# Kernel tuning notes

Measured on AMD Instinct MI355X. Metric: run time of the kernel, lower is better.

The kernel has to match this reference:

```python
import jax, jax.numpy as jnp
import numpy as np

N = 50000
E = 1000000
FN = 16
FE = 8
H = 64
DH = 64
LN_EPS = 1e-5


def _layernorm(x, g, b):
    mu = jnp.mean(x, axis=-1, keepdims=True)
    var = jnp.var(x, axis=-1, keepdims=True)
    return (x - mu) * jax.lax.rsqrt(var + LN_EPS) * g + b


def setup_inputs() -> dict:
    key = jax.random.key(0)
    ks = jax.random.split(key, 24)

    def w(k, i, o):
        return jax.random.normal(k, (i, o), jnp.float32) / np.sqrt(i).astype(np.float32)

    inp = {}
    inp["x"] = jax.random.normal(ks[0], (N, FN), jnp.float32)
    inp["edge_index"] = jax.random.randint(ks[1], (2, E), 0, N, dtype=jnp.int32)
    inp["edge_attr"] = jax.random.normal(ks[2], (E, FE), jnp.float32)
    # layer 0 (in_dim = FN, residual is a Linear since FN != H)
    inp["l0_lin_w"] = w(ks[3], FE, FN); inp["l0_lin_b"] = jnp.zeros((FN,), jnp.float32)
    inp["l0_w1"] = w(ks[4], FN, H);    inp["l0_b1"] = jnp.zeros((H,), jnp.float32)
    inp["l0_w2"] = w(ks[5], H, H);     inp["l0_b2"] = jnp.zeros((H,), jnp.float32)
    inp["l0_ln_g"] = jnp.ones((H,), jnp.float32); inp["l0_ln_b"] = jnp.zeros((H,), jnp.float32)
    inp["l0_res_w"] = w(ks[6], FN, H); inp["l0_res_b"] = jnp.zeros((H,), jnp.float32)
    # layers 1, 2 (in_dim = H, residual = identity)
    for li, base in ((1, 7), (2, 11)):
        inp[f"l{li}_lin_w"] = w(ks[base], FE, H);   inp[f"l{li}_lin_b"] = jnp.zeros((H,), jnp.float32)
        inp[f"l{li}_w1"] = w(ks[base + 1], H, H);   inp[f"l{li}_b1"] = jnp.zeros((H,), jnp.float32)
        inp[f"l{li}_w2"] = w(ks[base + 2], H, H);   inp[f"l{li}_b2"] = jnp.zeros((H,), jnp.float32)
        inp[f"l{li}_ln_g"] = jnp.ones((H,), jnp.float32)
        inp[f"l{li}_ln_b"] = jnp.zeros((H,), jnp.float32)
    D_IN = 4 * H + FE
    inp["dec_w1"] = w(ks[20], D_IN, DH);    inp["dec_b1"] = jnp.zeros((DH,), jnp.float32)
    inp["dec_w2"] = w(ks[21], DH, DH // 2); inp["dec_b2"] = jnp.zeros((DH // 2,), jnp.float32)
    inp["dec_w3"] = w(ks[22], DH // 2, 1);  inp["dec_b3"] = jnp.zeros((1,), jnp.float32)
    return inp


def _block(x, src, dst, edge_attr, lin_w, lin_b, w1, b1, w2, b2, ln_g, ln_b, res):
    # GINEConv: message = ReLU(x_src + Lin(edge_attr)); sum-aggregate at dst; eps=0
    msg = jax.nn.relu(x[src] + edge_attr @ lin_w + lin_b)      # (E, D_in)
    aggr = jax.ops.segment_sum(msg, dst, num_segments=N)       # (N, D_in)
    h = jax.nn.relu((x + aggr) @ w1 + b1) @ w2 + b2            # GIN nn MLP -> (N, H)
    h = jax.nn.relu(h)                                         # dropout inactive (eval)
    return _layernorm(h + res, ln_g, ln_b)


def reference(x, edge_index, edge_attr,
              l0_lin_w, l0_lin_b, l0_w1, l0_b1, l0_w2, l0_b2, l0_ln_g, l0_ln_b, l0_res_w, l0_res_b,
              l1_lin_w, l1_lin_b, l1_w1, l1_b1, l1_w2, l1_b2, l1_ln_g, l1_ln_b,
              l2_lin_w, l2_lin_b, l2_w1, l2_b1, l2_w2, l2_b2, l2_ln_g, l2_ln_b,
              dec_w1, dec_b1, dec_w2, dec_b2, dec_w3, dec_b3):
    src, dst = edge_index[0], edge_index[1]
    h = _block(x, src, dst, edge_attr, l0_lin_w, l0_lin_b, l0_w1, l0_b1, l0_w2, l0_b2,
               l0_ln_g, l0_ln_b, x @ l0_res_w + l0_res_b)
    h = _block(h, src, dst, edge_attr, l1_lin_w, l1_lin_b, l1_w1, l1_b1, l1_w2, l1_b2,
               l1_ln_g, l1_ln_b, h)
    h = _block(h, src, dst, edge_attr, l2_lin_w, l2_lin_b, l2_w1, l2_b1, l2_w2, l2_b2,
               l2_ln_g, l2_ln_b, h)
    hs, hd = h[src], h[dst]                                    # (E, H) each
    z = jnp.concatenate([hs, hd, jnp.abs(hs - hd), hs * hd, edge_attr], axis=-1)  # (E, 4H+FE)
    z = jax.nn.relu(z @ dec_w1 + dec_b1)
    z = jax.nn.relu(z @ dec_w2 + dec_b2)
    return (z @ dec_w3 + dec_b3)[:, 0]                         # (E,)
```

## Files before the change

### kernel.cpp

```cpp
#include <hip/hip_runtime.h>

#define NN 50000
#define NE 1000000

constexpr float LN_EPS = 1e-5f;

typedef short bf16x8 __attribute__((ext_vector_type(8)));
typedef float f32x4 __attribute__((ext_vector_type(4)));
typedef uint uvec4 __attribute__((ext_vector_type(4)));
typedef uint uvec2 __attribute__((ext_vector_type(2)));

__device__ inline uint cvtpk(float a, float b) {
  uint r;
  asm("v_cvt_pk_bf16_f32 %0, %1, %2" : "=v"(r) : "v"(a), "v"(b));
  return r;
}
__device__ inline ushort cvt1(float a) {
  uint r;
  asm("v_cvt_pk_bf16_f32 %0, %1, %1" : "=v"(r) : "v"(a));
  return (ushort)r;
}
__device__ inline float bflo(uint u) { union { uint x; float f; } v; v.x = u << 16; return v.f; }
__device__ inline float bfhi(uint u) { union { uint x; float f; } v; v.x = u & 0xffff0000u; return v.f; }

__global__ __launch_bounds__(256) void hist_kernel(const int* __restrict__ ei,
                                                   int* __restrict__ cnt) {
  int e = blockIdx.x * 256 + threadIdx.x;
  if (e < NE) atomicAdd(&cnt[ei[NE + e]], 1);
}

__global__ __launch_bounds__(256) void scan1_kernel(const int* __restrict__ cnt,
                                                    int* __restrict__ off,
                                                    int* __restrict__ bsum) {
  __shared__ int sh[256];
  int t = threadIdx.x;
  int idx = blockIdx.x * 256 + t;
  int v = (idx < NN) ? cnt[idx] : 0;
  sh[t] = v;
  __syncthreads();
  for (int o = 1; o < 256; o <<= 1) {
    int xv = (t >= o) ? sh[t - o] : 0;
    __syncthreads();
    sh[t] += xv;
    __syncthreads();
  }
  if (idx <= NN) off[idx] = sh[t] - v;
  if (t == 255) bsum[blockIdx.x] = sh[255];
}

__global__ __launch_bounds__(256) void scan2_kernel(int* __restrict__ bsum, int nb) {
  __shared__ int sh[256];
  int t = threadIdx.x;
  int v = (t < nb) ? bsum[t] : 0;
  sh[t] = v;
  __syncthreads();
  for (int o = 1; o < 256; o <<= 1) {
    int xv = (t >= o) ? sh[t - o] : 0;
    __syncthreads();
    sh[t] += xv;
    __syncthreads();
  }
  if (t < nb) bsum[t] = sh[t] - v;
}

__global__ __launch_bounds__(256) void scan3_kernel(int* __restrict__ off,
                                                    const int* __restrict__ bsum,
                                                    int* __restrict__ cnt) {
  int idx = blockIdx.x * 256 + threadIdx.x;
  if (idx <= NN) off[idx] += bsum[blockIdx.x];
  if (idx < NN) cnt[idx] = 0;
}

__global__ __launch_bounds__(256) void scatter_kernel(
    const int* __restrict__ ei, const float* __restrict__ ea,
    const int* __restrict__ off, int* __restrict__ cur,
    int* __restrict__ ipos, int* __restrict__ srcp, int* __restrict__ dstp,
    ushort* __restrict__ eapb) {
  int e = blockIdx.x * 256 + threadIdx.x;
  if (e < NE) {
    int d = ei[NE + e];
    int s = ei[e];
    int p = off[d] + atomicAdd(&cur[d], 1);
    ipos[e] = p;
    srcp[p] = s;
    dstp[p] = d;
    const float* eaf = ea + (size_t)e * 8;
    f32x4 e0 = *(const f32x4*)(eaf);
    f32x4 e1 = *(const f32x4*)(eaf + 4);
    uvec4 u;
    u.x = cvtpk(e0.x, e0.y);
    u.y = cvtpk(e0.z, e0.w);
    u.z = cvtpk(e1.x, e1.y);
    u.w = cvtpk(e1.z, e1.w);
    __builtin_nontemporal_store(u, (uvec4*)(eapb + (size_t)p * 8));
  }
}

__global__ __launch_bounds__(256) void unperm_kernel(const float* __restrict__ tmp,
                                                     const int* __restrict__ ipos,
                                                     float* __restrict__ out) {
  int e = blockIdx.x * 256 + threadIdx.x;
  if (e < NE) out[e] = tmp[ipos[e]];
}

__device__ inline float lane_layernorm(float r, float g, float b) {
  float s = r;
#pragma unroll
  for (int m = 32; m >= 1; m >>= 1) s += __shfl_xor(s, m);
  float mu = s * (1.f / 64.f);
  float dv = r - mu;
  float v = dv * dv;
#pragma unroll
  for (int m = 32; m >= 1; m >>= 1) v += __shfl_xor(v, m);
  float var = v * (1.f / 64.f);
  return dv * rsqrtf(var + LN_EPS) * g + b;
}

__global__ __launch_bounds__(256) void layer0_fused(
    const float* __restrict__ x, float* __restrict__ hout,
    ushort* __restrict__ houtbf,
    const ushort* __restrict__ eapb, const int* __restrict__ srcp,
    const int* __restrict__ off,
    const float* __restrict__ lw, const float* __restrict__ lb,
    const float* __restrict__ w1, const float* __restrict__ b1,
    const float* __restrict__ w2, const float* __restrict__ b2,
    const float* __restrict__ lng, const float* __restrict__ lnb,
    const float* __restrict__ rw, const float* __restrict__ rb) {
  int n = blockIdx.x * 4 + (threadIdx.x >> 6);
  int j = threadIdx.x & 63;
  int d = j & 15, slot = j >> 4;
  int start = off[n], end = off[n + 1];
  float lwv[8];
#pragma unroll
  for (int i = 0; i < 8; i++) lwv[i] = lw[i * 16 + d];
  float lbv = lb[d];
  float acc = 0.f;
  for (int base = start; base < end; base += 64) {
    int idx = base + j;
    int sl = (idx < end) ? srcp[idx] : 0;
    int c = min(end - base, 64);
    for (int i0 = 0; i0 < c; i0 += 4) {
      int i = i0 + slot;
      bool valid = i < c;
      int ii = i & 63;
      int s = __shfl(sl, ii);
      int pp = min(base + i0 + slot, NE - 1);
      float ev = bflo((uint)eapb[(size_t)pp * 8 + (d & 7)]);
      float xs = x[(size_t)s * 16 + d];
      float m = lbv + xs;
#pragma unroll
      for (int q = 0; q < 8; q++) m = fmaf(__shfl(ev, slot * 16 + q), lwv[q], m);
      m = fmaxf(m, 0.f);
      acc += valid ? m : 0.f;
    }
  }
  acc += __shfl_xor(acc, 16);
  acc += __shfl_xor(acc, 32);
  float xr = x[(size_t)n * 16 + d];
  float t = xr + acc;
  float q1 = b1[j];
#pragma unroll 4
  for (int k = 0; k < 16; k++) q1 = fmaf(__shfl(t, k), w1[k * 64 + j], q1);
  q1 = fmaxf(q1, 0.f);
  float h2 = b2[j];
  for (int k = 0; k < 64; k++) h2 = fmaf(__shfl(q1, k), w2[k * 64 + j], h2);
  h2 = fmaxf(h2, 0.f);
  float res = rb[j];
#pragma unroll 4
  for (int k = 0; k < 16; k++) res = fmaf(__shfl(xr, k), rw[k * 64 + j], res);
  float v = lane_layernorm(h2 + res, lng[j], lnb[j]);
  hout[(size_t)n * 64 + j] = v;
  houtbf[(size_t)n * 64 + j] = cvt1(v);
}

__device__ inline float edge8_msg(const ushort* __restrict__ hinb, int s, int j,
                                  uint ulo, uint uhi, uint vlo, uint vhi,
                                  const float* lwv, float lbv) {
  float hc = bflo((uint)hinb[(size_t)s * 64 + j]);
  float m = lbv + hc;
  m = fmaf(bflo(ulo), lwv[0], m);
  m = fmaf(bfhi(ulo), lwv[1], m);
  m = fmaf(bflo(uhi), lwv[2], m);
  m = fmaf(bfhi(uhi), lwv[3], m);
  m = fmaf(bflo(vlo), lwv[4], m);
  m = fmaf(bfhi(vlo), lwv[5], m);
  m = fmaf(bflo(vhi), lwv[6], m);
  m = fmaf(bfhi(vhi), lwv[7], m);
  return fmaxf(m, 0.f);
}

__global__ __launch_bounds__(256) void layer_fused(
    const ushort* __restrict__ hinb, const float* __restrict__ hinf,
    float* __restrict__ houtf, ushort* __restrict__ houtbf,
    const ushort* __restrict__ eapb, const int* __restrict__ srcp,
    const int* __restrict__ off,
    const float* __restrict__ lw, const float* __restrict__ lb,
    const float* __restrict__ w1, const float* __restrict__ b1,
    const float* __restrict__ w2, const float* __restrict__ b2,
    const float* __restrict__ lng, const float* __restrict__ lnb) {
  int n = blockIdx.x * 4 + (threadIdx.x >> 6);
  int j = threadIdx.x & 63;
  int start = __builtin_amdgcn_readfirstlane(off[n]);
  int end = __builtin_amdgcn_readfirstlane(off[n + 1]);
  float lwv[8];
#pragma unroll
  for (int i = 0; i < 8; i++) lwv[i] = lw[i * 64 + j];
  float lbv = lb[j];
  float acc = 0.f;
  int p = start;
  for (; p + 8 <= end; p += 8) {
    const uvec4* ip = (const uvec4*)(srcp + p);
    uvec4 I0 = __builtin_nontemporal_load(ip + 0);
    uvec4 I1 = __builtin_nontemporal_load(ip + 1);
    int s0 = __builtin_amdgcn_readfirstlane((int)I0.x);
    int s1 = __builtin_amdgcn_readfirstlane((int)I0.y);
    int s2 = __builtin_amdgcn_readfirstlane((int)I0.z);
    int s3 = __builtin_amdgcn_readfirstlane((int)I0.w);
    int s4 = __builtin_amdgcn_readfirstlane((int)I1.x);
    int s5 = __builtin_amdgcn_readfirstlane((int)I1.y);
    int s6 = __builtin_amdgcn_readfirstlane((int)I1.z);
    int s7 = __builtin_amdgcn_readfirstlane((int)I1.w);
    const uvec4* ep = (const uvec4*)(eapb + (size_t)p * 8);
    uint ua[8][4];
#pragma unroll
    for (int i = 0; i < 8; i++) {
      uvec4 E = __builtin_nontemporal_load(ep + i);
      ua[i][0] = __builtin_amdgcn_readfirstlane(E.x);
      ua[i][1] = __builtin_amdgcn_readfirstlane(E.y);
      ua[i][2] = __builtin_amdgcn_readfirstlane(E.z);
      ua[i][3] = __builtin_amdgcn_readfirstlane(E.w);
    }
    acc += edge8_msg(hinb, s0, j, ua[0][0], ua[0][1], ua[0][2], ua[0][3], lwv, lbv);
    acc += edge8_msg(hinb, s1, j, ua[1][0], ua[1][1], ua[1][2], ua[1][3], lwv, lbv);
    acc += edge8_msg(hinb, s2, j, ua[2][0], ua[2][1], ua[2][2], ua[2][3], lwv, lbv);
    acc += edge8_msg(hinb, s3, j, ua[3][0], ua[3][1], ua[3][2], ua[3][3], lwv, lbv);
    acc += edge8_msg(hinb, s4, j, ua[4][0], ua[4][1], ua[4][2], ua[4][3], lwv, lbv);
    acc += edge8_msg(hinb, s5, j, ua[5][0], ua[5][1], ua[5][2], ua[5][3], lwv, lbv);
    acc += edge8_msg(hinb, s6, j, ua[6][0], ua[6][1], ua[6][2], ua[6][3], lwv, lbv);
    acc += edge8_msg(hinb, s7, j, ua[7][0], ua[7][1], ua[7][2], ua[7][3], lwv, lbv);
  }
  for (; p < end; p++) {
    int s = __builtin_amdgcn_readfirstlane(srcp[p]);
    uvec4 E = __builtin_nontemporal_load((const uvec4*)(eapb + (size_t)p * 8));
    uint e0 = __builtin_amdgcn_readfirstlane(E.x);
    uint e1 = __builtin_amdgcn_readfirstlane(E.y);
    uint e2 = __builtin_amdgcn_readfirstlane(E.z);
    uint e3 = __builtin_amdgcn_readfirstlane(E.w);
    acc += edge8_msg(hinb, s, j, e0, e1, e2, e3, lwv, lbv);
  }
  float hv = __builtin_nontemporal_load(&hinf[(size_t)n * 64 + j]);
  float t = hv + acc;
  float q1 = b1[j];
  for (int k = 0; k < 64; k++) q1 = fmaf(__shfl(t, k), w1[k * 64 + j], q1);
  q1 = fmaxf(q1, 0.f);
  float h2 = b2[j];
  for (int k = 0; k < 64; k++) h2 = fmaf(__shfl(q1, k), w2[k * 64 + j], h2);
  h2 = fmaxf(h2, 0.f);
  float v = lane_layernorm(h2 + hv, lng[j], lnb[j]);
  if (houtf) houtf[(size_t)n * 64 + j] = v;
  houtbf[(size_t)n * 64 + j] = cvt1(v);
}

__global__ __launch_bounds__(256) void prep_kernel(
    const float* __restrict__ w1, const float* __restrict__ w2,
    ushort* __restrict__ w1f, ushort* __restrict__ w2f) {
  int t = blockIdx.x * 256 + threadIdx.x;
  if (t < 18432) {
    int j = t & 7, lane = (t >> 3) & 63, f = t >> 9;
    int k = (f >> 2) * 32 + ((lane >> 4) * 8) + j;
    int n = (f & 3) * 16 + (lane & 15);
    float v = (k < 264) ? w1[k * 64 + n] : 0.f;
    w1f[t] = cvt1(v);
  } else {
    int t2 = t - 18432;
    int j = t2 & 7, lane = (t2 >> 3) & 63, f = t2 >> 9;
    int k = (f >> 1) * 32 + ((lane >> 4) * 8) + j;
    int n = (f & 1) * 16 + (lane & 15);
    w2f[t2] = cvt1(w2[k * 32 + n]);
  }
}

#define YS 72
#define NBLK 15625
#define BPX 1954

__device__ inline void absmul(bf16x8 a, bf16x8 b, bf16x8& dd, bf16x8& pp) {
  union U { bf16x8 v; uvec4 u; } ua, ub, ud, up;
  ua.v = a; ub.v = b;
#pragma unroll
  for (int i = 0; i < 4; i++) {
    float a0 = bflo(ua.u[i]), a1 = bfhi(ua.u[i]);
    float b0 = bflo(ub.u[i]), b1 = bfhi(ub.u[i]);
    ud.u[i] = cvtpk(fabsf(a0 - b0), fabsf(a1 - b1));
    up.u[i] = cvtpk(a0 * b0, a1 * b1);
  }
  dd = ud.v; pp = up.v;
}

__global__ __launch_bounds__(128, 4) void decoder_kernel(
    const ushort* __restrict__ hb,
    const int* __restrict__ srcp, const int* __restrict__ dstp,
    const ushort* __restrict__ eapb,
    const ushort* __restrict__ w1f, const ushort* __restrict__ w2f,
    const float* __restrict__ b1, const float* __restrict__ b2,
    const float* __restrict__ w3, const float* __restrict__ b3,
    float* __restrict__ tmp) {
  __shared__ ushort ybuf[2][32 * YS];
  const int w = threadIdx.x >> 6, l = threadIdx.x & 63;
  const int sub = l & 15, quad = l >> 4;
  int bb = (blockIdx.x & 7) * BPX + (blockIdx.x >> 3);
  if (bb >= NBLK) return;
  const int g = bb * 2 + w;
  ushort* Y = ybuf[w];

  int s32 = __builtin_nontemporal_load(&srcp[g * 32 + (l & 31)]);
  int d32 = __builtin_nontemporal_load(&dstp[g * 32 + (l & 31)]);

  bf16x8 alo[2], ahi[2], blo[2], bhi[2];
#pragma unroll
  for (int m = 0; m < 2; m++) {
    int sA = __shfl(s32, m * 16 + sub);
    int dA = __shfl(d32, m * 16 + sub);
    const ushort* pa = hb + (size_t)sA * 64 + quad * 8;
    const ushort* pb = hb + (size_t)dA * 64 + quad * 8;
    alo[m] = *(const bf16x8*)pa;
    ahi[m] = *(const bf16x8*)(pa + 32);
    blo[m] = *(const bf16x8*)pb;
    bhi[m] = *(const bf16x8*)(pb + 32);
  }
  bf16x8 eaf0 = (bf16x8){0, 0, 0, 0, 0, 0, 0, 0};
  bf16x8 eaf1 = (bf16x8){0, 0, 0, 0, 0, 0, 0, 0};
  if (quad == 0) {
    eaf0 = *(const bf16x8*)&eapb[((size_t)g * 32 + sub) * 8];
    eaf1 = *(const bf16x8*)&eapb[((size_t)g * 32 + 16 + sub) * 8];
  }

  float b1v[4];
#pragma unroll
  for (int t = 0; t < 4; t++) b1v[t] = b1[t * 16 + sub];
  float b2v0 = b2[sub], b2v1 = b2[16 + sub];
  float w3v0 = w3[sub], w3v1 = w3[16 + sub];
  float b3v = b3[0];

  f32x4 acc[2][4];
#pragma unroll
  for (int m = 0; m < 2; m++)
#pragma unroll
    for (int t = 0; t < 4; t++) acc[m][t] = (f32x4){0.f, 0.f, 0.f, 0.f};

#define MF(sB, f0, f1)                                                        \
  {                                                                           \
    _Pragma("unroll") for (int t = 0; t < 4; t++) {                           \
      bf16x8 bfv = ((const bf16x8*)w1f)[((sB)*4 + t) * 64 + l];               \
      acc[0][t] = __builtin_amdgcn_mfma_f32_16x16x32_bf16(f0, bfv, acc[0][t], \
                                                          0, 0, 0);           \
      acc[1][t] = __builtin_amdgcn_mfma_f32_16x16x32_bf16(f1, bfv, acc[1][t], \
                                                          0, 0, 0);           \
    }                                                                         \
  }

  {
    bf16x8 dlo0, plo0, dlo1, plo1;
    absmul(alo[0], blo[0], dlo0, plo0);
    absmul(alo[1], blo[1], dlo1, plo1);
    MF(0, alo[0], alo[1]);
    MF(2, blo[0], blo[1]);
    MF(4, dlo0, dlo1);
    MF(6, plo0, plo1);
  }
  {
    bf16x8 dhi0, phi0, dhi1, phi1;
    absmul(ahi[0], bhi[0], dhi0, phi0);
    absmul(ahi[1], bhi[1], dhi1, phi1);
    MF(1, ahi[0], ahi[1]);
    MF(3, bhi[0], bhi[1]);
    MF(5, dhi0, dhi1);
    MF(7, phi0, phi1);
  }
  MF(8, eaf0, eaf1);
#undef MF

#pragma unroll
  for (int m = 0; m < 2; m++)
#pragma unroll
    for (int t = 0; t < 4; t++)
#pragma unroll
      for (int r = 0; r < 4; r++)
        Y[(m * 16 + quad * 4 + r) * YS + t * 16 + sub] =
            cvt1(fmaxf(acc[m][t][r] + b1v[t], 0.f));

  bf16x8 w2frag[4];
#pragma unroll
  for (int f = 0; f < 4; f++) w2frag[f] = ((const bf16x8*)w2f)[f * 64 + l];
  f32x4 acc2[2][2];
#pragma unroll
  for (int m = 0; m < 2; m++) {
    acc2[m][0] = (f32x4){0.f, 0.f, 0.f, 0.f};
    acc2[m][1] = (f32x4){0.f, 0.f, 0.f, 0.f};
#pragma unroll
    for (int ks = 0; ks < 2; ks++) {
      bf16x8 ya = *(const bf16x8*)&Y[(m * 16 + sub) * YS + ks * 32 + quad * 8];
      acc2[m][0] = __builtin_amdgcn_mfma_f32_16x16x32_bf16(ya, w2frag[ks * 2 + 0],
                                                           acc2[m][0], 0, 0, 0);
      acc2[m][1] = __builtin_amdgcn_mfma_f32_16x16x32_bf16(ya, w2frag[ks * 2 + 1],
                                                           acc2[m][1], 0, 0, 0);
    }
  }
#pragma unroll
  for (int m = 0; m < 2; m++)
#pragma unroll
    for (int r = 0; r < 4; r++) {
      float o = fmaxf(acc2[m][0][r] + b2v0, 0.f) * w3v0 +
                fmaxf(acc2[m][1][r] + b2v1, 0.f) * w3v1;
      o += __shfl_xor(o, 1);
      o += __shfl_xor(o, 2);
      o += __shfl_xor(o, 4);
      o += __shfl_xor(o, 8);
      if (sub == 0) tmp[g * 32 + m * 16 + quad * 4 + r] = o + b3v;
    }
}

extern "C" void kernel_launch(void* const* d_in, const int* in_sizes, int n_in,
                              void* d_out, int out_size, void* d_ws, size_t ws_size,
                              hipStream_t stream) {
  const float* x = (const float*)d_in[0];
  const int* ei = (const int*)d_in[1];
  const float* ea = (const float*)d_in[2];
  const float* l0_lin_w = (const float*)d_in[3];
  const float* l0_lin_b = (const float*)d_in[4];
  const float* l0_w1 = (const float*)d_in[5];
  const float* l0_b1 = (const float*)d_in[6];
  const float* l0_w2 = (const float*)d_in[7];
  const float* l0_b2 = (const float*)d_in[8];
  const float* l0_ln_g = (const float*)d_in[9];
  const float* l0_ln_b = (const float*)d_in[10];
  const float* l0_res_w = (const float*)d_in[11];
  const float* l0_res_b = (const float*)d_in[12];
  const float* dec_w1 = (const float*)d_in[29];
  const float* dec_b1 = (const float*)d_in[30];
  const float* dec_w2 = (const float*)d_in[31];
  const float* dec_b2 = (const float*)d_in[32];
  const float* dec_w3 = (const float*)d_in[33];
  const float* dec_b3 = (const float*)d_in[34];

  float* h_a = (float*)d_ws;
  float* h_b = h_a + (size_t)NN * 64;
  ushort* hbA = (ushort*)(h_b + (size_t)NN * 64);
  ushort* hbB = hbA + (size_t)NN * 64;
  int* ipos = (int*)(hbB + (size_t)NN * 64);
  int* srcp = ipos + NE;
  int* dstp = srcp + NE;
  float* tmp = (float*)(dstp + NE);
  int* off = (int*)(tmp + NE);
  int* cnt = off + (NN + 1);
  int* bsum = cnt + NN;
  ushort* w1f = (ushort*)(bsum + 256);
  ushort* w2f = w1f + 18432;
  ushort* eapb = w2f + 2048;

  const int EB = (NE + 255) / 256;
  const int SB = (NN + 256) / 256;

  hipMemsetAsync(cnt, 0, (size_t)NN * sizeof(int), stream);
  hist_kernel<<<EB, 256, 0, stream>>>(ei, cnt);
  scan1_kernel<<<SB, 256, 0, stream>>>(cnt, off, bsum);
  scan2_kernel<<<1, 256, 0, stream>>>(bsum, SB);
  scan3_kernel<<<SB, 256, 0, stream>>>(off, bsum, cnt);
  scatter_kernel<<<EB, 256, 0, stream>>>(ei, ea, off, cnt, ipos, srcp, dstp, eapb);

  layer0_fused<<<NN / 4, 256, 0, stream>>>(x, h_a, hbA, eapb, srcp, off,
                                           l0_lin_w, l0_lin_b, l0_w1, l0_b1,
                                           l0_w2, l0_b2, l0_ln_g, l0_ln_b,
                                           l0_res_w, l0_res_b);
  layer_fused<<<NN / 4, 256, 0, stream>>>(hbA, h_a, h_b, hbB, eapb, srcp, off,
                                          (const float*)d_in[13], (const float*)d_in[14],
                                          (const float*)d_in[15], (const float*)d_in[16],
                                          (const float*)d_in[17], (const float*)d_in[18],
                                          (const float*)d_in[19], (const float*)d_in[20]);
  layer_fused<<<NN / 4, 256, 0, stream>>>(hbB, h_b, (float*)nullptr, hbA, eapb, srcp, off,
                                          (const float*)d_in[21], (const float*)d_in[22],
                                          (const float*)d_in[23], (const float*)d_in[24],
                                          (const float*)d_in[25], (const float*)d_in[26],
                                          (const float*)d_in[27], (const float*)d_in[28]);

  prep_kernel<<<80, 256, 0, stream>>>(dec_w1, dec_w2, w1f, w2f);
  decoder_kernel<<<8 * BPX, 128, 0, stream>>>(hbA, srcp, dstp, eapb,
                                              w1f, w2f, dec_b1, dec_b2,
                                              dec_w3, dec_b3, tmp);
  unperm_kernel<<<EB, 256, 0, stream>>>(tmp, ipos, (float*)d_out);
}
```

Baseline: 617.1 us.

## Split GINE layers into aggregation and MFMA-based node MLP kernels

Layers 1 and 2 were a single fused kernel where each wavefront ran the 64x64 MLP per node with shuffles and scalar FMAs. They are now split into an aggregation kernel that writes per-node sums to a float scratch buffer, and a separate MLP kernel. The MLP kernel processes 32 nodes per wave using bf16 MFMA with a hi/lo split (three products) to keep close to fp32 accuracy, followed by LayerNorm. This removes the shuffle-bound per-node matmul at the cost of an extra round trip of 50000x64 floats through memory, two more launches, and a weight-prep kernel.

```diff
diff --git a/kernel.cpp b/kernel.cpp
--- a/kernel.cpp
+++ b/kernel.cpp
@@ -189,15 +189,11 @@
   return fmaxf(m, 0.f);
 }
 
-__global__ __launch_bounds__(256) void layer_fused(
-    const ushort* __restrict__ hinb, const float* __restrict__ hinf,
-    float* __restrict__ houtf, ushort* __restrict__ houtbf,
+__global__ __launch_bounds__(256) void aggr_kernel(
+    const ushort* __restrict__ hinb, float* __restrict__ tout,
     const ushort* __restrict__ eapb, const int* __restrict__ srcp,
     const int* __restrict__ off,
-    const float* __restrict__ lw, const float* __restrict__ lb,
-    const float* __restrict__ w1, const float* __restrict__ b1,
-    const float* __restrict__ w2, const float* __restrict__ b2,
-    const float* __restrict__ lng, const float* __restrict__ lnb) {
+    const float* __restrict__ lw, const float* __restrict__ lb) {
   int n = blockIdx.x * 4 + (threadIdx.x >> 6);
   int j = threadIdx.x & 63;
   int start = __builtin_amdgcn_readfirstlane(off[n]);
@@ -248,17 +244,7 @@
     uint e3 = __builtin_amdgcn_readfirstlane(E.w);
     acc += edge8_msg(hinb, s, j, e0, e1, e2, e3, lwv, lbv);
   }
-  float hv = __builtin_nontemporal_load(&hinf[(size_t)n * 64 + j]);
-  float t = hv + acc;
-  float q1 = b1[j];
-  for (int k = 0; k < 64; k++) q1 = fmaf(__shfl(t, k), w1[k * 64 + j], q1);
-  q1 = fmaxf(q1, 0.f);
-  float h2 = b2[j];
-  for (int k = 0; k < 64; k++) h2 = fmaf(__shfl(q1, k), w2[k * 64 + j], h2);
-  h2 = fmaxf(h2, 0.f);
-  float v = lane_layernorm(h2 + hv, lng[j], lnb[j]);
-  if (houtf) houtf[(size_t)n * 64 + j] = v;
-  houtbf[(size_t)n * 64 + j] = cvt1(v);
+  tout[(size_t)n * 64 + j] = acc;
 }
 
 __global__ __launch_bounds__(256) void prep_kernel(
@@ -277,6 +263,200 @@
     int k = (f >> 1) * 32 + ((lane >> 4) * 8) + j;
     int n = (f & 1) * 16 + (lane & 15);
     w2f[t2] = cvt1(w2[k * 32 + n]);
+  }
+}
+
+__global__ __launch_bounds__(256) void prep_mlpw(
+    const float* __restrict__ w1a, const float* __restrict__ w2a,
+    const float* __restrict__ w1b, const float* __restrict__ w2b,
+    ushort* __restrict__ out) {
+  int t = blockIdx.x * 256 + threadIdx.x;
+  int layer = t >> 13, wsel = (t >> 12) & 1, idx = t & 4095;
+  const float* w = layer ? (wsel ? w2b : w1b) : (wsel ? w2a : w1a);
+  int j = idx & 7, lane = (idx >> 3) & 63, f = idx >> 9;
+  int k = (f >> 2) * 32 + ((lane >> 4) * 8) + j;
+  int n = (f & 3) * 16 + (lane & 15);
+  float v = w[k * 64 + n];
+  ushort h = cvt1(v);
+  float r = v - bflo((uint)h);
+  ushort lo = cvt1(r);
+  int base = layer * 16384 + wsel * 8192;
+  out[base + idx] = h;
+  out[base + 4096 + idx] = lo;
+}
+
+#define YS2 68
+
+__global__ __launch_bounds__(128) void mlp_kernel(
+    const float* __restrict__ tacc, const float* __restrict__ hinf,
+    float* __restrict__ houtf, ushort* __restrict__ houtbf,
+    const ushort* __restrict__ wf,
+    const float* __restrict__ b1, const float* __restrict__ b2,
+    const float* __restrict__ lng, const float* __restrict__ lnb) {
+  __shared__ float ybuf[2][32 * YS2];
+  const int w = threadIdx.x >> 6, l = threadIdx.x & 63;
+  const int sub = l & 15, quad = l >> 4;
+  const int wid = blockIdx.x * 2 + w;
+  const int r0 = wid * 32;
+  if (r0 >= NN) return;
+  float* Y = ybuf[w];
+
+  const bf16x8* w1h = (const bf16x8*)wf;
+  const bf16x8* w1l = (const bf16x8*)(wf + 4096);
+  const bf16x8* w2h = (const bf16x8*)(wf + 8192);
+  const bf16x8* w2l = (const bf16x8*)(wf + 12288);
+
+  union UF { uvec4 u; bf16x8 v; };
+
+  bf16x8 Ahi[2][2], Alo[2][2];
+#pragma unroll
+  for (int m = 0; m < 2; m++) {
+    int row = min(r0 + m * 16 + sub, NN - 1);
+    const float* pt = tacc + (size_t)row * 64 + quad * 8;
+    const float* ph = hinf + (size_t)row * 64 + quad * 8;
+#pragma unroll
+    for (int ks = 0; ks < 2; ks++) {
+      f32x4 t0 = *(const f32x4*)(pt + ks * 32);
+      f32x4 t1 = *(const f32x4*)(pt + ks * 32 + 4);
+      f32x4 h0 = *(const f32x4*)(ph + ks * 32);
+      f32x4 h1 = *(const f32x4*)(ph + ks * 32 + 4);
+      t0 += h0;
+      t1 += h1;
+      UF uh, ul;
+      uh.u.x = cvtpk(t0.x, t0.y);
+      uh.u.y = cvtpk(t0.z, t0.w);
+      uh.u.z = cvtpk(t1.x, t1.y);
+      uh.u.w = cvtpk(t1.z, t1.w);
+      ul.u.x = cvtpk(t0.x - bflo(uh.u.x), t0.y - bfhi(uh.u.x));
+      ul.u.y = cvtpk(t0.z - bflo(uh.u.y), t0.w - bfhi(uh.u.y));
+      ul.u.z = cvtpk(t1.x - bflo(uh.u.z), t1.y - bfhi(uh.u.z));
+      ul.u.w = cvtpk(t1.z - bflo(uh.u.w), t1.w - bfhi(uh.u.w));
+      Ahi[m][ks] = uh.v;
+      Alo[m][ks] = ul.v;
+    }
+  }
+
+  f32x4 c1[2][4];
+#pragma unroll
+  for (int m = 0; m < 2; m++)
+#pragma unroll
+    for (int nb = 0; nb < 4; nb++) c1[m][nb] = (f32x4){0.f, 0.f, 0.f, 0.f};
+#pragma unroll
+  for (int nb = 0; nb < 4; nb++) {
+#pragma unroll
+    for (int ks = 0; ks < 2; ks++) {
+      bf16x8 bh = w1h[(ks * 4 + nb) * 64 + l];
+      bf16x8 bl = w1l[(ks * 4 + nb) * 64 + l];
+      c1[0][nb] = __builtin_amdgcn_mfma_f32_16x16x32_bf16(Ahi[0][ks], bh, c1[0][nb], 0, 0, 0);
+      c1[1][nb] = __builtin_amdgcn_mfma_f32_16x16x32_bf16(Ahi[1][ks], bh, c1[1][nb], 0, 0, 0);
+      c1[0][nb] = __builtin_amdgcn_mfma_f32_16x16x32_bf16(Alo[0][ks], bh, c1[0][nb], 0, 0, 0);
+      c1[1][nb] = __builtin_amdgcn_mfma_f32_16x16x32_bf16(Alo[1][ks], bh, c1[1][nb], 0, 0, 0);
+      c1[0][nb] = __builtin_amdgcn_mfma_f32_16x16x32_bf16(Ahi[0][ks], bl, c1[0][nb], 0, 0, 0);
+      c1[1][nb] = __builtin_amdgcn_mfma_f32_16x16x32_bf16(Ahi[1][ks], bl, c1[1][nb], 0, 0, 0);
+    }
+  }
+
+  float b1v[4];
+#pragma unroll
+  for (int nb = 0; nb < 4; nb++) b1v[nb] = b1[nb * 16 + sub];
+#pragma unroll
+  for (int m = 0; m < 2; m++)
+#pragma unroll
+    for (int nb = 0; nb < 4; nb++)
+#pragma unroll
+      for (int r = 0; r < 4; r++)
+        Y[(m * 16 + quad * 4 + r) * YS2 + nb * 16 + sub] =
+            fmaxf(c1[m][nb][r] + b1v[nb], 0.f);
+
+  bf16x8 Qhi[2][2], Qlo[2][2];
+#pragma unroll
+  for (int m = 0; m < 2; m++) {
+#pragma unroll
+    for (int ks = 0; ks < 2; ks++) {
+      const float* py = &Y[(m * 16 + sub) * YS2 + ks * 32 + quad * 8];
+      f32x4 q0 = *(const f32x4*)py;
+      f32x4 q1 = *(const f32x4*)(py + 4);
+      UF uh, ul;
+      uh.u.x = cvtpk(q0.x, q0.y);
+      uh.u.y = cvtpk(q0.z, q0.w);
+      uh.u.z = cvtpk(q1.x, q1.y);
+      uh.u.w = cvtpk(q1.z, q1.w);
+      ul.u.x = cvtpk(q0.x - bflo(uh.u.x), q0.y - bfhi(uh.u.x));
+      ul.u.y = cvtpk(q0.z - bflo(uh.u.y), q0.w - bfhi(uh.u.y));
+      ul.u.z = cvtpk(q1.x - bflo(uh.u.z), q1.y - bfhi(uh.u.z));
+      ul.u.w = cvtpk(q1.z - bflo(uh.u.w), q1.w - bfhi(uh.u.w));
+      Qhi[m][ks] = uh.v;
+      Qlo[m][ks] = ul.v;
+    }
+  }
+
+  f32x4 c2[2][4];
+#pragma unroll
+  for (int m = 0; m < 2; m++)
+#pragma unroll
+    for (int nb = 0; nb < 4; nb++) c2[m][nb] = (f32x4){0.f, 0.f, 0.f, 0.f};
+#pragma unroll
+  for (int nb = 0; nb < 4; nb++) {
+#pragma unroll
+    for (int ks = 0; ks < 2; ks++) {
+      bf16x8 bh = w2h[(ks * 4 + nb) * 64 + l];
+      bf16x8 bl = w2l[(ks * 4 + nb) * 64 + l];
+      c2[0][nb] = __builtin_amdgcn_mfma_f32_16x16x32_bf16(Qhi[0][ks], bh, c2[0][nb], 0, 0, 0);
+      c2[1][nb] = __builtin_amdgcn_mfma_f32_16x16x32_bf16(Qhi[1][ks], bh, c2[1][nb], 0, 0, 0);
+      c2[0][nb] = __builtin_amdgcn_mfma_f32_16x16x32_bf16(Qlo[0][ks], bh, c2[0][nb], 0, 0, 0);
+      c2[1][nb] = __builtin_amdgcn_mfma_f32_16x16x32_bf16(Qlo[1][ks], bh, c2[1][nb], 0, 0, 0);
+      c2[0][nb] = __builtin_amdgcn_mfma_f32_16x16x32_bf16(Qhi[0][ks], bl, c2[0][nb], 0, 0, 0);
+      c2[1][nb] = __builtin_amdgcn_mfma_f32_16x16x32_bf16(Qhi[1][ks], bl, c2[1][nb], 0, 0, 0);
+    }
+  }
+
+  float b2v[4], lngv[4], lnbv[4];
+#pragma unroll
+  for (int nb = 0; nb < 4; nb++) {
+    b2v[nb] = b2[nb * 16 + sub];
+    lngv[nb] = lng[nb * 16 + sub];
+    lnbv[nb] = lnb[nb * 16 + sub];
+  }
+#pragma unroll
+  for (int m = 0; m < 2; m++) {
+#pragma unroll
+    for (int r = 0; r < 4; r++) {
+      int node = r0 + m * 16 + quad * 4 + r;
+      int nc = min(node, NN - 1);
+      float vp[4];
+      float s = 0.f;
+#pragma unroll
+      for (int nb = 0; nb < 4; nb++) {
+        vp[nb] = fmaxf(c2[m][nb][r] + b2v[nb], 0.f) +
+                 hinf[(size_t)nc * 64 + nb * 16 + sub];
+        s += vp[nb];
+      }
+      s += __shfl_xor(s, 1);
+      s += __shfl_xor(s, 2);
+      s += __shfl_xor(s, 4);
+      s += __shfl_xor(s, 8);
+      float mu = s * (1.f / 64.f);
+      float vv = 0.f;
+      float dv[4];
+#pragma unroll
+      for (int nb = 0; nb < 4; nb++) {
+        dv[nb] = vp[nb] - mu;
+        vv += dv[nb] * dv[nb];
+      }
+      vv += __shfl_xor(vv, 1);
+      vv += __shfl_xor(vv, 2);
+      vv += __shfl_xor(vv, 4);
+      vv += __shfl_xor(vv, 8);
+      float rstd = rsqrtf(vv * (1.f / 64.f) + LN_EPS);
+      if (node < NN) {
+#pragma unroll
+        for (int nb = 0; nb < 4; nb++) {
+          float o = dv[nb] * rstd * lngv[nb] + lnbv[nb];
+          if (houtf) houtf[(size_t)node * 64 + nb * 16 + sub] = o;
+          houtbf[(size_t)node * 64 + nb * 16 + sub] = cvt1(o);
+        }
+      }
+    }
   }
 }
 
@@ -457,9 +637,12 @@
   ushort* w1f = (ushort*)(bsum + 256);
   ushort* w2f = w1f + 18432;
   ushort* eapb = w2f + 2048;
+  ushort* wmlp = eapb + (size_t)NE * 8;
+  float* tacc = (float*)(wmlp + 32768);
 
   const int EB = (NE + 255) / 256;
   const int SB = (NN + 256) / 256;
+  const int MB = ((NN + 31) / 32 + 1) / 2;
 
   hipMemsetAsync(cnt, 0, (size_t)NN * sizeof(int), stream);
   hist_kernel<<<EB, 256, 0, stream>>>(ei, cnt);
@@ -467,21 +650,26 @@
   scan2_kernel<<<1, 256, 0, stream>>>(bsum, SB);
   scan3_kernel<<<SB, 256, 0, stream>>>(off, bsum, cnt);
   scatter_kernel<<<EB, 256, 0, stream>>>(ei, ea, off, cnt, ipos, srcp, dstp, eapb);
+  prep_mlpw<<<64, 256, 0, stream>>>((const float*)d_in[15], (const float*)d_in[17],
+                                    (const float*)d_in[23], (const float*)d_in[25],
+                                    wmlp);
 
   layer0_fused<<<NN / 4, 256, 0, stream>>>(x, h_a, hbA, eapb, srcp, off,
                                            l0_lin_w, l0_lin_b, l0_w1, l0_b1,
                                            l0_w2, l0_b2, l0_ln_g, l0_ln_b,
                                            l0_res_w, l0_res_b);
-  layer_fused<<<NN / 4, 256, 0, stream>>>(hbA, h_a, h_b, hbB, eapb, srcp, off,
-                                          (const float*)d_in[13], (const float*)d_in[14],
-                                          (const float*)d_in[15], (const float*)d_in[16],
-                                          (const float*)d_in[17], (const float*)d_in[18],
-                                          (const float*)d_in[19], (const float*)d_in[20]);
-  layer_fused<<<NN / 4, 256, 0, stream>>>(hbB, h_b, (float*)nullptr, hbA, eapb, srcp, off,
-                                          (const float*)d_in[21], (const float*)d_in[22],
-                                          (const float*)d_in[23], (const float*)d_in[24],
-                                          (const float*)d_in[25], (const float*)d_in[26],
-                                          (const float*)d_in[27], (const float*)d_in[28]);
+  aggr_kernel<<<NN / 4, 256, 0, stream>>>(hbA, tacc, eapb, srcp, off,
+                                          (const float*)d_in[13],
+                                          (const float*)d_in[14]);
+  mlp_kernel<<<MB, 128, 0, stream>>>(tacc, h_a, h_b, hbB, wmlp,
+                                     (const float*)d_in[16], (const float*)d_in[18],
+                                     (const float*)d_in[19], (const float*)d_in[20]);
+  aggr_kernel<<<NN / 4, 256, 0, stream>>>(hbB, tacc, eapb, srcp, off,
+                                          (const float*)d_in[21],
+                                          (const float*)d_in[22]);
+  mlp_kernel<<<MB, 128, 0, stream>>>(tacc, h_b, (float*)nullptr, hbA, wmlp + 16384,
+                                     (const float*)d_in[24], (const float*)d_in[26],
+                                     (const float*)d_in[27], (const float*)d_in[28]);
 
   prep_kernel<<<80, 256, 0, stream>>>(dec_w1, dec_w2, w1f, w2f);
   decoder_kernel<<<8 * BPX, 128, 0, stream>>>(hbA, srcp, dstp, eapb,
```

Measured after the change: 572.6 us. 1.08x faster.
